# Optimization experiments

Hardware: AMD Instinct MI355X
Metric: run time of the kernel (lower is better)

## Reference

```python
import jax, jax.numpy as jnp
import numpy as np

WIN_SIZE = 11
SIGMA = 1.5
WEIGHTS = np.array([0.0448, 0.2856, 0.3001, 0.2363, 0.1333], dtype=np.float32)
K1, K2 = 0.01, 0.03
DATA_RANGE = 255.0
C1 = (K1 * DATA_RANGE) ** 2
C2 = (K2 * DATA_RANGE) ** 2
N_SCALES = 5


def _gauss1d():
    coords = np.arange(WIN_SIZE, dtype=np.float32) - WIN_SIZE // 2
    g = np.exp(-(coords ** 2) / (2.0 * SIGMA ** 2))
    g /= g.sum()
    return jnp.asarray(g, dtype=jnp.float32)


def _blur(x, g):
    # separable depthwise gaussian blur, VALID padding (matches pytorch_msssim)
    C = x.shape[1]
    wh = jnp.tile(g.reshape(1, 1, 1, WIN_SIZE), (C, 1, 1, 1))
    wv = jnp.tile(g.reshape(1, 1, WIN_SIZE, 1), (C, 1, 1, 1))
    dn = ('NCHW', 'OIHW', 'NCHW')
    x = jax.lax.conv_general_dilated(x, wh, (1, 1), 'VALID', dimension_numbers=dn, feature_group_count=C)
    x = jax.lax.conv_general_dilated(x, wv, (1, 1), 'VALID', dimension_numbers=dn, feature_group_count=C)
    return x


def _ssim(X, Y, g):
    mu1 = _blur(X, g)
    mu2 = _blur(Y, g)
    mu1_sq = mu1 * mu1
    mu2_sq = mu2 * mu2
    mu1_mu2 = mu1 * mu2
    sigma1_sq = _blur(X * X, g) - mu1_sq
    sigma2_sq = _blur(Y * Y, g) - mu2_sq
    sigma12 = _blur(X * Y, g) - mu1_mu2
    cs_map = (2.0 * sigma12 + C2) / (sigma1_sq + sigma2_sq + C2)
    ssim_map = ((2.0 * mu1_mu2 + C1) / (mu1_sq + mu2_sq + C1)) * cs_map
    return ssim_map.mean(axis=(2, 3)), cs_map.mean(axis=(2, 3))  # [B,C] each


def _avg_pool2(x):
    # avg_pool2d kernel=2 stride=2; H,W chosen even at every scale so padding=0
    return jax.lax.reduce_window(x, 0.0, jax.lax.add, (1, 1, 2, 2), (1, 1, 2, 2), 'VALID') / 4.0


def setup_inputs() -> dict:
    key = jax.random.key(0)
    k1, k2 = jax.random.split(key)
    shape = (32, 3, 384, 384)
    prediction = jax.random.uniform(k1, shape, dtype=jnp.float32) * DATA_RANGE
    truth = jax.random.uniform(k2, shape, dtype=jnp.float32) * DATA_RANGE
    return {"prediction": prediction, "truth": truth}


def reference(prediction, truth):
    g = _gauss1d()
    w = jnp.asarray(WEIGHTS)
    X, Y = prediction, truth
    mcs = []
    for i in range(N_SCALES):
        ssim_pc, cs = _ssim(X, Y, g)
        if i < N_SCALES - 1:
            mcs.append(jax.nn.relu(cs))
            X = _avg_pool2(X)
            Y = _avg_pool2(Y)
    vals = jnp.stack(mcs + [jax.nn.relu(ssim_pc)], axis=0)  # [5,B,C]
    ms_ssim_val = jnp.prod(vals ** w.reshape(-1, 1, 1), axis=0)  # [B,C]
    return 1.0 - ms_ssim_val.mean()
```

## Files before the change

### kernel.cpp

```cpp
#include <hip/hip_runtime.h>
#include <math.h>


namespace {

constexpr int NIMG = 96;
constexpr float C1c = 6.5025f;
constexpr float C2c = 58.5225f;

__device__ constexpr float GW[11] = {
    0.00102838f, 0.00759875f, 0.03600077f, 0.10936070f, 0.21300553f,
    0.26601172f,
    0.21300553f, 0.10936070f, 0.03600077f, 0.00759875f, 0.00102838f};

__device__ __forceinline__ float wshl1(float v) {
  return __int_as_float(__builtin_amdgcn_mov_dpp(
      __float_as_int(v), 0x130, 0xF, 0xF, true));
}

struct SPtrs {
  const float* x[5];
  const float* y[5];
};

__global__ __launch_bounds__(256) void ssim_all(SPtrs sp,
                                                float* __restrict__ acc) {
  __shared__ float red[2][4];

  const int tile = blockIdx.x;
  int s;
  if (tile < 84) s = 0;
  else if (tile < 108) s = 1;
  else if (tile < 114) s = 2;
  else if (tile < 116) s = 3;
  else s = 4;
  const int tstart[5] = {0, 84, 108, 114, 116};
  const int HH[5] = {384, 192, 96, 48, 24};
  const int TXc[5] = {7, 4, 2, 1, 1};
  const int lt = tile - tstart[s];
  const int H = HH[s], W = H, OH = H - 10, OW = W - 10;
  const int tx = lt % TXc[s], ty = lt / TXc[s];
  const int img = blockIdx.z;
  const float* Xi = sp.x[s] + (size_t)img * H * W;
  const float* Yi = sp.y[s] + (size_t)img * H * W;

  const int t = threadIdx.x;
  const int lane = t & 63, wv = t >> 6;
  const int col = tx * 54 + lane;
  const int cin = col < W - 1 ? col : W - 1;
  const int row0 = ty * 32 + wv * 8;

  float a0[8] = {}, a1[8] = {}, a2[8] = {}, a3[8] = {}, a4[8] = {};
#pragma unroll
  for (int j = 0; j < 18; ++j) {
    int rin = row0 + j;
    rin = rin < H - 1 ? rin : H - 1;
    float x = Xi[(size_t)rin * W + cin];
    float y = Yi[(size_t)rin * W + cin];
    float xx = x * x, yy = y * y, xy = x * y;
#pragma unroll
    for (int i = 0; i < 8; ++i) {
      const int k = j - i;
      if (k >= 0 && k <= 10) {
        const float wt = GW[k];
        a0[i] += wt * x;
        a1[i] += wt * y;
        a2[i] += wt * xx;
        a3[i] += wt * yy;
        a4[i] += wt * xy;
      }
    }
  }

  const bool colok = (lane < 54) && (col < OW);
  float ssim_s = 0.f, cs_s = 0.f;
#pragma unroll
  for (int i = 0; i < 8; ++i) {
    float t0 = a0[i], t1 = a1[i], t2 = a2[i], t3 = a3[i], t4 = a4[i];
    float b0 = GW[0] * t0, b1 = GW[0] * t1, b2 = GW[0] * t2,
          b3 = GW[0] * t3, b4 = GW[0] * t4;
#pragma unroll
    for (int k = 1; k <= 10; ++k) {
      t0 = wshl1(t0); b0 += GW[k] * t0;
      t1 = wshl1(t1); b1 += GW[k] * t1;
      t2 = wshl1(t2); b2 += GW[k] * t2;
      t3 = wshl1(t3); b3 += GW[k] * t3;
      t4 = wshl1(t4); b4 += GW[k] * t4;
    }
    if (colok && (row0 + i < OH)) {
      float mu1 = b0, mu2 = b1;
      float mu1sq = mu1 * mu1, mu2sq = mu2 * mu2, mu12 = mu1 * mu2;
      float s1 = b2 - mu1sq, s2v = b3 - mu2sq, s12 = b4 - mu12;
      float cs = (2.f * s12 + C2c) * __builtin_amdgcn_rcpf(s1 + s2v + C2c);
      float ss = (2.f * mu12 + C1c) *
                 __builtin_amdgcn_rcpf(mu1sq + mu2sq + C1c) * cs;
      cs_s += cs;
      ssim_s += ss;
    }
  }

#pragma unroll
  for (int off = 32; off > 0; off >>= 1) {
    ssim_s += __shfl_down(ssim_s, off);
    cs_s += __shfl_down(cs_s, off);
  }
  if (lane == 0) { red[0][wv] = ssim_s; red[1][wv] = cs_s; }
  __syncthreads();
  if (t == 0) {
    atomicAdd(&acc[(2 * s + 0) * NIMG + img],
              red[0][0] + red[0][1] + red[0][2] + red[0][3]);
    atomicAdd(&acc[(2 * s + 1) * NIMG + img],
              red[1][0] + red[1][1] + red[1][2] + red[1][3]);
  }
}

__global__ __launch_bounds__(256) void pyramid_kernel(
    const float* __restrict__ X, const float* __restrict__ Y,
    float* __restrict__ x1, float* __restrict__ y1,
    float* __restrict__ x2, float* __restrict__ y2,
    float* __restrict__ x3, float* __restrict__ y3,
    float* __restrict__ x4, float* __restrict__ y4,
    float* __restrict__ acc) {
  const int img = blockIdx.y;
  const int t = threadIdx.x;
  if (blockIdx.x == 0 && img == 0) {
    for (int i = t; i < 10 * NIMG; i += 256) acc[i] = 0.f;
  }
  const int wv = t >> 6, lane = t & 63;
  const int tidx = blockIdx.x * 4 + wv;
  const int tx = tidx % 24, ty = tidx / 24;
  const int r = lane >> 3, c = lane & 7;

  const float* src[2] = {X + (size_t)img * 384 * 384,
                         Y + (size_t)img * 384 * 384};
  float* o1[2] = {x1 + (size_t)img * 192 * 192, y1 + (size_t)img * 192 * 192};
  float* o2[2] = {x2 + (size_t)img * 96 * 96,   y2 + (size_t)img * 96 * 96};
  float* o3[2] = {x3 + (size_t)img * 48 * 48,   y3 + (size_t)img * 48 * 48};
  float* o4[2] = {x4 + (size_t)img * 24 * 24,   y4 + (size_t)img * 24 * 24};

#pragma unroll
  for (int ch = 0; ch < 2; ++ch) {
    const float* S = src[ch];
    int gr = ty * 16 + 2 * r, gc = tx * 16 + 2 * c;
    float2 u = *(const float2*)&S[(size_t)gr * 384 + gc];
    float2 v = *(const float2*)&S[(size_t)(gr + 1) * 384 + gc];
    float l1 = 0.25f * (u.x + u.y + v.x + v.y);
    o1[ch][(size_t)(ty * 8 + r) * 192 + tx * 8 + c] = l1;

    float l2 = l1 + __shfl_xor(l1, 1);
    l2 = 0.25f * (l2 + __shfl_xor(l2, 8));
    if ((r & 1) == 0 && (c & 1) == 0)
      o2[ch][(size_t)(ty * 4 + (r >> 1)) * 96 + tx * 4 + (c >> 1)] = l2;

    float l3 = l2 + __shfl_xor(l2, 2);
    l3 = 0.25f * (l3 + __shfl_xor(l3, 16));
    if ((r & 3) == 0 && (c & 3) == 0)
      o3[ch][(size_t)(ty * 2 + (r >> 2)) * 48 + tx * 2 + (c >> 2)] = l3;

    float l4 = l3 + __shfl_xor(l3, 4);
    l4 = 0.25f * (l4 + __shfl_xor(l4, 32));
    if (lane == 0) o4[ch][(size_t)ty * 24 + tx] = l4;
  }
}

__global__ void final_kernel(const float* __restrict__ acc,
                             float* __restrict__ out) {
  __shared__ float prods[NIMG];
  const float wts[5] = {0.0448f, 0.2856f, 0.3001f, 0.2363f, 0.1333f};
  const float inv_npix[5] = {1.f / (374.f * 374.f), 1.f / (182.f * 182.f),
                             1.f / (86.f * 86.f),  1.f / (38.f * 38.f),
                             1.f / (14.f * 14.f)};
  int t = threadIdx.x;
  if (t < NIMG) {
    float p = 1.f;
#pragma unroll
    for (int s = 0; s < 5; ++s) {
      float sum = (s < 4) ? acc[(s * 2 + 1) * NIMG + t]
                          : acc[(s * 2 + 0) * NIMG + t];
      float m = sum * inv_npix[s];
      m = m > 0.f ? m : 0.f;
      p *= powf(m, wts[s]);
    }
    prods[t] = p;
  }
  __syncthreads();
  if (t == 0) {
    float s = 0.f;
    for (int i = 0; i < NIMG; ++i) s += prods[i];
    out[0] = 1.f - s / (float)NIMG;
  }
}

}

extern "C" void kernel_launch(void* const* d_in, const int* in_sizes, int n_in,
                              void* d_out, int out_size, void* d_ws,
                              size_t ws_size, hipStream_t stream) {
  const float* X0 = (const float*)d_in[0];
  const float* Y0 = (const float*)d_in[1];
  float* out = (float*)d_out;
  float* ws = (float*)d_ws;

  const size_t L1 = (size_t)NIMG * 192 * 192;
  const size_t L2 = (size_t)NIMG * 96 * 96;
  const size_t L3 = (size_t)NIMG * 48 * 48;
  const size_t L4 = (size_t)NIMG * 24 * 24;

  float* x1 = ws;
  float* x2 = x1 + L1;
  float* x3 = x2 + L2;
  float* x4 = x3 + L3;
  float* y1 = x4 + L4;
  float* y2 = y1 + L1;
  float* y3 = y2 + L2;
  float* y4 = y3 + L3;
  float* acc = y4 + L4;

  pyramid_kernel<<<dim3(144, NIMG), dim3(256), 0, stream>>>(
      X0, Y0, x1, y1, x2, y2, x3, y3, x4, y4, acc);

  SPtrs sp;
  sp.x[0] = X0; sp.x[1] = x1; sp.x[2] = x2; sp.x[3] = x3; sp.x[4] = x4;
  sp.y[0] = Y0; sp.y[1] = y1; sp.y[2] = y2; sp.y[3] = y3; sp.y[4] = y4;

  ssim_all<<<dim3(117, 1, NIMG), dim3(256), 0, stream>>>(sp, acc);

  final_kernel<<<dim3(1), dim3(128), 0, stream>>>(acc, out);
}
```

Baseline: 249.8 us.

## Blur sum/difference images to cut moment blurs from five to four, packed FMA

```diff
diff --git a/kernel.cpp b/kernel.cpp
--- a/kernel.cpp
+++ b/kernel.cpp
@@ -5,17 +5,34 @@
 namespace {
 
 constexpr int NIMG = 96;
-constexpr float C1c = 6.5025f;
-constexpr float C2c = 58.5225f;
+constexpr float TWO_C1 = 13.005f;
+constexpr float TWO_C2 = 117.045f;
 
 __device__ constexpr float GW[11] = {
     0.00102838f, 0.00759875f, 0.03600077f, 0.10936070f, 0.21300553f,
     0.26601172f,
     0.21300553f, 0.10936070f, 0.03600077f, 0.00759875f, 0.00102838f};
 
+typedef float f2 __attribute__((ext_vector_type(2)));
+
+__device__ __forceinline__ f2 pk(f2 a, f2 b, f2 c) {
+#if __has_builtin(__builtin_elementwise_fma)
+  return __builtin_elementwise_fma(a, b, c);
+#else
+  return a * b + c;
+#endif
+}
+
 __device__ __forceinline__ float wshl1(float v) {
   return __int_as_float(__builtin_amdgcn_mov_dpp(
       __float_as_int(v), 0x130, 0xF, 0xF, true));
+}
+
+__device__ __forceinline__ f2 wshl1v(f2 v) {
+  f2 r;
+  r.x = wshl1(v.x);
+  r.y = wshl1(v.y);
+  return r;
 }
 
 struct SPtrs {
@@ -43,6 +60,7 @@
   const int img = blockIdx.z;
   const float* Xi = sp.x[s] + (size_t)img * H * W;
   const float* Yi = sp.y[s] + (size_t)img * H * W;
+  const bool base = (s == 0);
 
   const int t = threadIdx.x;
   const int lane = t & 63, wv = t >> 6;
@@ -50,24 +68,24 @@
   const int cin = col < W - 1 ? col : W - 1;
   const int row0 = ty * 32 + wv * 8;
 
-  float a0[8] = {}, a1[8] = {}, a2[8] = {}, a3[8] = {}, a4[8] = {};
+  f2 A[8] = {}, B[8] = {};
 #pragma unroll
   for (int j = 0; j < 18; ++j) {
     int rin = row0 + j;
     rin = rin < H - 1 ? rin : H - 1;
-    float x = Xi[(size_t)rin * W + cin];
-    float y = Yi[(size_t)rin * W + cin];
-    float xx = x * x, yy = y * y, xy = x * y;
+    float a = Xi[(size_t)rin * W + cin];
+    float b = Yi[(size_t)rin * W + cin];
+    f2 P;
+    P.x = base ? a + b : a;
+    P.y = base ? a - b : b;
+    f2 Q = P * P;
 #pragma unroll
     for (int i = 0; i < 8; ++i) {
       const int k = j - i;
       if (k >= 0 && k <= 10) {
-        const float wt = GW[k];
-        a0[i] += wt * x;
-        a1[i] += wt * y;
-        a2[i] += wt * xx;
-        a3[i] += wt * yy;
-        a4[i] += wt * xy;
+        const f2 wt = GW[k];
+        A[i] = pk(wt, P, A[i]);
+        B[i] = pk(wt, Q, B[i]);
       }
     }
   }
@@ -76,26 +94,26 @@
   float ssim_s = 0.f, cs_s = 0.f;
 #pragma unroll
   for (int i = 0; i < 8; ++i) {
-    float t0 = a0[i], t1 = a1[i], t2 = a2[i], t3 = a3[i], t4 = a4[i];
-    float b0 = GW[0] * t0, b1 = GW[0] * t1, b2 = GW[0] * t2,
-          b3 = GW[0] * t3, b4 = GW[0] * t4;
+    f2 tA = A[i], tB = B[i];
+    f2 bA = ((f2)GW[0]) * tA;
+    f2 bB = ((f2)GW[0]) * tB;
 #pragma unroll
     for (int k = 1; k <= 10; ++k) {
-      t0 = wshl1(t0); b0 += GW[k] * t0;
-      t1 = wshl1(t1); b1 += GW[k] * t1;
-      t2 = wshl1(t2); b2 += GW[k] * t2;
-      t3 = wshl1(t3); b3 += GW[k] * t3;
-      t4 = wshl1(t4); b4 += GW[k] * t4;
+      const f2 wt = GW[k];
+      tA = wshl1v(tA); bA = pk(wt, tA, bA);
+      tB = wshl1v(tB); bB = pk(wt, tB, bB);
     }
     if (colok && (row0 + i < OH)) {
-      float mu1 = b0, mu2 = b1;
-      float mu1sq = mu1 * mu1, mu2sq = mu2 * mu2, mu12 = mu1 * mu2;
-      float s1 = b2 - mu1sq, s2v = b3 - mu2sq, s12 = b4 - mu12;
-      float cs = (2.f * s12 + C2c) * __builtin_amdgcn_rcpf(s1 + s2v + C2c);
-      float ss = (2.f * mu12 + C1c) *
-                 __builtin_amdgcn_rcpf(mu1sq + mu2sq + C1c) * cs;
+      float m2u = bA.x * bA.x, m2w = bA.y * bA.y;
+      float Pm = m2u - m2w;
+      float Qm = m2u + m2w;
+      float Am = bB.x - bB.y;
+      float Bm = bB.x + bB.y;
+      float cs = (Am - Pm + TWO_C2) *
+                 __builtin_amdgcn_rcpf(Bm - Qm + TWO_C2);
+      float l = (Pm + TWO_C1) * __builtin_amdgcn_rcpf(Qm + TWO_C1);
       cs_s += cs;
-      ssim_s += ss;
+      ssim_s += l * cs;
     }
   }
 
@@ -116,10 +134,10 @@
 
 __global__ __launch_bounds__(256) void pyramid_kernel(
     const float* __restrict__ X, const float* __restrict__ Y,
-    float* __restrict__ x1, float* __restrict__ y1,
-    float* __restrict__ x2, float* __restrict__ y2,
-    float* __restrict__ x3, float* __restrict__ y3,
-    float* __restrict__ x4, float* __restrict__ y4,
+    float* __restrict__ u1, float* __restrict__ w1,
+    float* __restrict__ u2, float* __restrict__ w2,
+    float* __restrict__ u3, float* __restrict__ w3,
+    float* __restrict__ u4, float* __restrict__ w4,
     float* __restrict__ acc) {
   const int img = blockIdx.y;
   const int t = threadIdx.x;
@@ -131,20 +149,26 @@
   const int tx = tidx % 24, ty = tidx / 24;
   const int r = lane >> 3, c = lane & 7;
 
-  const float* src[2] = {X + (size_t)img * 384 * 384,
-                         Y + (size_t)img * 384 * 384};
-  float* o1[2] = {x1 + (size_t)img * 192 * 192, y1 + (size_t)img * 192 * 192};
-  float* o2[2] = {x2 + (size_t)img * 96 * 96,   y2 + (size_t)img * 96 * 96};
-  float* o3[2] = {x3 + (size_t)img * 48 * 48,   y3 + (size_t)img * 48 * 48};
-  float* o4[2] = {x4 + (size_t)img * 24 * 24,   y4 + (size_t)img * 24 * 24};
+  const float* Xs = X + (size_t)img * 384 * 384;
+  const float* Ys = Y + (size_t)img * 384 * 384;
+  float* o1[2] = {u1 + (size_t)img * 192 * 192, w1 + (size_t)img * 192 * 192};
+  float* o2[2] = {u2 + (size_t)img * 96 * 96,   w2 + (size_t)img * 96 * 96};
+  float* o3[2] = {u3 + (size_t)img * 48 * 48,   w3 + (size_t)img * 48 * 48};
+  float* o4[2] = {u4 + (size_t)img * 24 * 24,   w4 + (size_t)img * 24 * 24};
+
+  int gr = ty * 16 + 2 * r, gc = tx * 16 + 2 * c;
+  float2 xu = *(const float2*)&Xs[(size_t)gr * 384 + gc];
+  float2 xv = *(const float2*)&Xs[(size_t)(gr + 1) * 384 + gc];
+  float2 yu = *(const float2*)&Ys[(size_t)gr * 384 + gc];
+  float2 yv = *(const float2*)&Ys[(size_t)(gr + 1) * 384 + gc];
+  float l1x = 0.25f * (xu.x + xu.y + xv.x + xv.y);
+  float l1y = 0.25f * (yu.x + yu.y + yv.x + yv.y);
+  float ch0 = l1x + l1y, ch1 = l1x - l1y;
+  float lv[2] = {ch0, ch1};
 
 #pragma unroll
   for (int ch = 0; ch < 2; ++ch) {
-    const float* S = src[ch];
-    int gr = ty * 16 + 2 * r, gc = tx * 16 + 2 * c;
-    float2 u = *(const float2*)&S[(size_t)gr * 384 + gc];
-    float2 v = *(const float2*)&S[(size_t)(gr + 1) * 384 + gc];
-    float l1 = 0.25f * (u.x + u.y + v.x + v.y);
+    float l1 = lv[ch];
     o1[ch][(size_t)(ty * 8 + r) * 192 + tx * 8 + c] = l1;
 
     float l2 = l1 + __shfl_xor(l1, 1);
@@ -206,22 +230,22 @@
   const size_t L3 = (size_t)NIMG * 48 * 48;
   const size_t L4 = (size_t)NIMG * 24 * 24;
 
-  float* x1 = ws;
-  float* x2 = x1 + L1;
-  float* x3 = x2 + L2;
-  float* x4 = x3 + L3;
-  float* y1 = x4 + L4;
-  float* y2 = y1 + L1;
-  float* y3 = y2 + L2;
-  float* y4 = y3 + L3;
-  float* acc = y4 + L4;
+  float* u1 = ws;
+  float* u2 = u1 + L1;
+  float* u3 = u2 + L2;
+  float* u4 = u3 + L3;
+  float* w1 = u4 + L4;
+  float* w2 = w1 + L1;
+  float* w3 = w2 + L2;
+  float* w4 = w3 + L3;
+  float* acc = w4 + L4;
 
   pyramid_kernel<<<dim3(144, NIMG), dim3(256), 0, stream>>>(
-      X0, Y0, x1, y1, x2, y2, x3, y3, x4, y4, acc);
+      X0, Y0, u1, w1, u2, w2, u3, w3, u4, w4, acc);
 
   SPtrs sp;
-  sp.x[0] = X0; sp.x[1] = x1; sp.x[2] = x2; sp.x[3] = x3; sp.x[4] = x4;
-  sp.y[0] = Y0; sp.y[1] = y1; sp.y[2] = y2; sp.y[3] = y3; sp.y[4] = y4;
+  sp.x[0] = X0; sp.x[1] = u1; sp.x[2] = u2; sp.x[3] = u3; sp.x[4] = u4;
+  sp.y[0] = Y0; sp.y[1] = w1; sp.y[2] = w2; sp.y[3] = w3; sp.y[4] = w4;
 
   ssim_all<<<dim3(117, 1, NIMG), dim3(256), 0, stream>>>(sp, acc);
 
```

New measurement: 238.9 us. 1.05x faster.
